# Kernel optimization log

Hardware: AMD Instinct MI355X
Metric: run time of the kernel (lower is better)

The kernel has to match this reference:

```python
import jax, jax.numpy as jnp
import numpy as np

B, C, H, W = 8, 256, 64, 64
CR = C // 4  # reduced channels for Q/K


def setup_inputs() -> dict:
    key = jax.random.key(0)
    ks = jax.random.split(key, 6)
    return {
        "source": jax.random.normal(ks[0], (B, C, H, W), dtype=jnp.float32),
        "guidance": jax.random.normal(ks[1], (B, C, H, W), dtype=jnp.float32),
        "Wq": jax.random.normal(ks[2], (CR, C), dtype=jnp.float32) * 0.02,
        "Wk": jax.random.normal(ks[3], (CR, C), dtype=jnp.float32) * 0.02,
        "Wv": jax.random.normal(ks[4], (C, C), dtype=jnp.float32) * 0.02,
        "bv": jax.random.normal(ks[5], (C,), dtype=jnp.float32) * 0.02,
        "gamma": jnp.zeros((1,), dtype=jnp.float32),
    }


def reference(source, guidance, Wq, Wk, Wv, bv, gamma):
    b, c, h, w = source.shape
    n = h * w
    src = source.reshape(b, c, n)       # [B,C,N]
    gui = guidance.reshape(b, c, n)     # [B,C,N]
    # 1x1 convs == per-pixel linear projections over channels
    Q = jnp.einsum('qc,bcn->bqn', Wq, src)                 # [B,CR,N]
    K = jnp.einsum('qc,bcn->bqn', Wk, gui)                 # [B,CR,N]
    V = jnp.einsum('vc,bcn->bvn', Wv, gui) + bv[None, :, None]  # [B,C,N]
    # energy[b,n,m] = sum_q Q[b,q,n] K[b,q,m]  (unscaled)
    energy = jnp.einsum('bqn,bqm->bnm', Q, K)              # [B,N,N]
    attn = jax.nn.softmax(energy, axis=-1)                 # softmax over keys m
    # out[b,c,n] = sum_m V[b,c,m] attn[b,n,m]
    out = jnp.einsum('bcm,bnm->bcn', V, attn)              # [B,C,N]
    return gamma[0] * out.reshape(b, c, h, w) + source
```

## Files before the change

kernel.cpp:

```cpp
#include <hip/hip_runtime.h>
#include <hip/hip_bf16.h>
#include <stdint.h>


#define B_ 8
#define C_ 256
#define N_ 4096
#define CR_ 64

typedef unsigned short u16;
typedef __attribute__((ext_vector_type(8))) __bf16 bf16x8;
typedef __attribute__((ext_vector_type(4))) float f32x4;
typedef __attribute__((ext_vector_type(16))) float f32x16;

__device__ __forceinline__ u16 f2bf(float f) {
  union { float f; unsigned int u; } v; v.f = f;
  unsigned int r = (v.u + 0x7fffu + ((v.u >> 16) & 1u)) >> 16;
  return (u16)r;
}
__device__ __forceinline__ unsigned int cvtpk(float a, float b) {
  unsigned int r;
  asm("v_cvt_pk_bf16_f32 %0, %1, %2" : "=v"(r) : "v"(a), "v"(b));
  return r;
}

typedef __attribute__((address_space(1))) const unsigned int gu32_t;
typedef __attribute__((address_space(3))) unsigned int lu32_t;
__device__ __forceinline__ void gll16(const void* g, void* l) {
  __builtin_amdgcn_global_load_lds((gu32_t*)g, (lu32_t*)l, 16, 0, 0);
}

__global__ __launch_bounds__(256) void wprep_kernel(
    const float* __restrict__ Wq, const float* __restrict__ Wk,
    const float* __restrict__ Wv, u16* __restrict__ Wb)
{
  const int i = (blockIdx.x * 256 + threadIdx.x) * 4;
  const int row = i >> 8;
  float4 v;
  float s = 1.0f;
  if (row < 64)       { v = *(const float4*)(Wq + i); s = 1.44269504f; }
  else if (row < 128) { v = *(const float4*)(Wk + i - 64 * 256); }
  else                { v = *(const float4*)(Wv + i - 128 * 256); }
  u16* o = Wb + i;
  o[0] = f2bf(v.x * s); o[1] = f2bf(v.y * s);
  o[2] = f2bf(v.z * s); o[3] = f2bf(v.w * s);
}

#define TSTR 266
#define LOAD_TILE(INP, BB, PX0) do {                                         \
    const int p4_ = (t & 15) * 4, r_ = t >> 4;                               \
    const float* ip_ = (INP) + (size_t)(BB) * C_ * N_ + (PX0) + p4_;         \
    for (int k = 0; k < 16; ++k) {                                           \
      const int c_ = r_ + k * 16;                                            \
      float4 v_ = *(const float4*)(ip_ + (size_t)c_ * N_);                   \
      Tl[(p4_ + 0) * TSTR + c_] = f2bf(v_.x);                                \
      Tl[(p4_ + 1) * TSTR + c_] = f2bf(v_.y);                                \
      Tl[(p4_ + 2) * TSTR + c_] = f2bf(v_.z);                                \
      Tl[(p4_ + 3) * TSTR + c_] = f2bf(v_.w);                                \
    }                                                                        \
  } while (0)

__global__ __launch_bounds__(256) void projqkv_kernel(
    const float* __restrict__ src, const float* __restrict__ gui,
    const u16* __restrict__ Wb, const float* __restrict__ bv,
    u16* __restrict__ Qb, u16* __restrict__ Kb, u16* __restrict__ VF)
{
  __shared__ u16 Tl[64 * TSTR];
  const int t = threadIdx.x, lane = t & 63, wave = t >> 6;
  const int lg = lane >> 4, lm = lane & 15;
  const int b = blockIdx.y;
  const int l31 = lane & 31, hi2 = lane >> 5;
  const f32x4 z4 = {0.f, 0.f, 0.f, 0.f};

  if (blockIdx.z == 0) {
    LOAD_TILE(src, b, blockIdx.x * 64);
    __syncthreads();

    f32x4 acc[4];
#pragma unroll
    for (int i = 0; i < 4; ++i) acc[i] = z4;
    for (int ks = 0; ks < 8; ++ks) {
      bf16x8 wf = *(const bf16x8*)(Wb + (wave * 16 + lm) * C_ + ks * 32 + lg * 8);
#pragma unroll
      for (int ni = 0; ni < 4; ++ni) {
        bf16x8 pf = *(const bf16x8*)(&Tl[(ni * 16 + lm) * TSTR + ks * 32 + lg * 8]);
        acc[ni] = __builtin_amdgcn_mfma_f32_16x16x32_bf16(wf, pf, acc[ni], 0, 0, 0);
      }
    }
    __syncthreads();
#pragma unroll
    for (int ni = 0; ni < 4; ++ni)
#pragma unroll
      for (int rp = 0; rp < 2; ++rp)
        *(unsigned int*)&Tl[(ni * 16 + lm) * 72 + wave * 16 + lg * 4 + rp * 2] =
            cvtpk(acc[ni][rp * 2], acc[ni][rp * 2 + 1]);
    __syncthreads();
    u16* op = Qb + (size_t)(b * 64 + blockIdx.x) * 4096 + lane * 8;
#pragma unroll
    for (int fi = 0; fi < 2; ++fi) {
      const int f = wave * 2 + fi, sub = f >> 2, db = f & 3;
      *(uint4*)(op + f * 512) =
          *(const uint4*)(&Tl[(sub * 32 + l31) * 72 + db * 16 + hi2 * 8]);
    }
  } else {
    LOAD_TILE(gui, b, blockIdx.x * 64);
    __syncthreads();

    const u16* Wk64 = Wb + 64 * 256;
    const u16* Wv0  = Wb + 128 * 256 + (size_t)(wave * 64) * 256;
    f32x4 acck[4];
    f32x4 accv[4][4];
#pragma unroll
    for (int i = 0; i < 4; ++i) {
      acck[i] = z4;
#pragma unroll
      for (int j = 0; j < 4; ++j) accv[i][j] = z4;
    }

    for (int ks = 0; ks < 8; ++ks) {
      bf16x8 pf[4];
#pragma unroll
      for (int ni = 0; ni < 4; ++ni)
        pf[ni] = *(const bf16x8*)(&Tl[(ni * 16 + lm) * TSTR + ks * 32 + lg * 8]);
      bf16x8 kwf = *(const bf16x8*)(Wk64 + (wave * 16 + lm) * C_ + ks * 32 + lg * 8);
#pragma unroll
      for (int ni = 0; ni < 4; ++ni)
        acck[ni] = __builtin_amdgcn_mfma_f32_16x16x32_bf16(kwf, pf[ni], acck[ni], 0, 0, 0);
#pragma unroll
      for (int mi = 0; mi < 4; ++mi) {
        bf16x8 vwf = *(const bf16x8*)(Wv0 + (mi * 16 + lm) * C_ + ks * 32 + lg * 8);
#pragma unroll
        for (int ni = 0; ni < 4; ++ni)
          accv[mi][ni] = __builtin_amdgcn_mfma_f32_16x16x32_bf16(vwf, pf[ni], accv[mi][ni], 0, 0, 0);
      }
    }

    f32x4 bq[4];
#pragma unroll
    for (int mi = 0; mi < 4; ++mi)
      bq[mi] = *(const f32x4*)(bv + wave * 64 + mi * 16 + lg * 4);

    __syncthreads();

    u16* tw = Tl + wave * 32 * 72;
    const int half = wave >> 1;
    u16* vo = VF + (((size_t)(b * 64 + blockIdx.x)) * 2 + half) * 8192;
#pragma unroll
    for (int vh = 0; vh < 2; ++vh) {
#pragma unroll
      for (int mi = 0; mi < 2; ++mi)
#pragma unroll
        for (int ni = 0; ni < 4; ++ni)
#pragma unroll
          for (int r = 0; r < 4; ++r)
            tw[(mi * 16 + lg * 4 + r) * 72 + ni * 16 + lm] =
                f2bf(accv[vh * 2 + mi][ni][r] + bq[vh * 2 + mi][r]);
      const int cf = (wave & 1) * 2 + vh;
#pragma unroll
      for (int kblk = 0; kblk < 4; ++kblk)
        *(uint4*)(vo + (cf * 4 + kblk) * 512 + lane * 8) =
            *(const uint4*)(&tw[l31 * 72 + kblk * 16 + hi2 * 8]);
    }

    __syncthreads();
#pragma unroll
    for (int ni = 0; ni < 4; ++ni)
#pragma unroll
      for (int rp = 0; rp < 2; ++rp)
        *(unsigned int*)&Tl[(ni * 16 + lm) * 72 + wave * 16 + lg * 4 + rp * 2] =
            cvtpk(acck[ni][rp * 2], acck[ni][rp * 2 + 1]);
    __syncthreads();
    u16* op = Kb + (size_t)(b * 64 + blockIdx.x) * 4096 + lane * 8;
#pragma unroll
    for (int fi = 0; fi < 2; ++fi) {
      const int f = wave * 2 + fi, sub = f >> 2, db = f & 3;
      *(uint4*)(op + f * 512) =
          *(const uint4*)(&Tl[(sub * 32 + l31) * 72 + db * 16 + hi2 * 8]);
    }
  }
}

#define VB1 16384
#define PB  32768

__global__ __launch_bounds__(256, 4) void attn_kernel(
    const u16* __restrict__ Qb, const u16* __restrict__ Kb, const u16* __restrict__ VF,
    const float* __restrict__ source, const float* __restrict__ gamma,
    float* __restrict__ out)
{
  __shared__ uint4 smem4[2560];
  char* smem = (char*)smem4;

  const int bid = blockIdx.x;
  const int b = bid & 7;
  const int idx = bid >> 3;
  const int qt = idx & 63;
  const int half = idx >> 6;

  const int t = threadIdx.x;
  const int lane = t & 63;
  const int wave = t >> 6;
  const int qw = wave & 1;
  const int wc = wave >> 1;
  const int l31 = lane & 31;
  const int hi = lane >> 5;
  const int q0 = qt * 64;

  bf16x8 aq[4];
  {
    const u16* qp = Qb + ((size_t)(b * 64 + qt)) * 4096 + (qw * 4) * 512 + lane * 8;
#pragma unroll
    for (int db = 0; db < 4; ++db) aq[db] = *(const bf16x8*)(qp + db * 512);
  }

  const u16* KbT = Kb + (size_t)b * (64 * 4096);
  const char* VFb = (const char*)VF + ((size_t)(b * 128 + half)) * 16384;

  f32x16 acc[2];
#pragma unroll
  for (int c2 = 0; c2 < 2; ++c2)
#pragma unroll
    for (int r = 0; r < 16; ++r) acc[c2][r] = 0.f;
  float lpart = 0.f;

  bf16x8 kC[4];
  char* pmy0 = smem + PB + (size_t)((qw * 4 + wc * 2 + 0) << 10) + lane * 16;
  char* pmy1 = smem + PB + (size_t)((qw * 4 + wc * 2 + 1) << 10) + lane * 16;
  const char* pfr0 = smem + PB + (size_t)((qw * 4 + (1 - wc) * 2 + 0) << 10) + lane * 16;
  const char* pfr1 = smem + PB + (size_t)((qw * 4 + (1 - wc) * 2 + 1) << 10) + lane * 16;

#define STAGEV(KTILE, VOFF) do {                                             \
    const char* vs_ = VFb + (size_t)(KTILE) * 32768 + t * 16;                \
    _Pragma("unroll")                                                        \
    for (int i = 0; i < 4; ++i)                                              \
      gll16(vs_ + i * 4096, smem + (VOFF) + wave * 1024 + i * 4096);         \
  } while (0)

#define LOADK(KT) do {                                                       \
    const u16* kp_ = KbT + (size_t)(KT) * 4096 + wc * 2048 + lane * 8;       \
    _Pragma("unroll")                                                        \
    for (int f = 0; f < 4; ++f)                                              \
      kC[f] = *(const bf16x8*)(kp_ + f * 512);                               \
  } while (0)

#define PACK(SF, O8, DST) do {                                               \
    unsigned uA_ = cvtpk(SF[(O8) + 0], SF[(O8) + 1]);                        \
    unsigned vA_ = cvtpk(SF[(O8) + 2], SF[(O8) + 3]);                        \
    unsigned uB_ = cvtpk(SF[(O8) + 4], SF[(O8) + 5]);                        \
    unsigned vB_ = cvtpk(SF[(O8) + 6], SF[(O8) + 7]);                        \
    asm("v_permlane32_swap_b32 %0, %1" : "+v"(uA_), "+v"(uB_));              \
    asm("v_permlane32_swap_b32 %0, %1" : "+v"(vA_), "+v"(vB_));              \
    uint4 pw_; pw_.x = uA_; pw_.y = vA_; pw_.z = uB_; pw_.w = vB_;           \
    __builtin_memcpy(&(DST), &pw_, 16);                                      \
  } while (0)

#define PVK(KBLK, PB8, VCUR) do {                                            \
    __builtin_amdgcn_s_setprio(1);                                           \
    _Pragma("unroll")                                                        \
    for (int c2 = 0; c2 < 2; ++c2) {                                         \
      bf16x8 vf_ = *(const bf16x8*)(smem + (VCUR) +                          \
          (((wc * 2 + c2) * 4 + (KBLK)) << 10) + lane * 16);                 \
      acc[c2] = __builtin_amdgcn_mfma_f32_32x32x16_bf16(vf_, PB8, acc[c2], 0, 0, 0); \
    }                                                                        \
    __builtin_amdgcn_s_setprio(0);                                           \
  } while (0)

#define ITER(KT, VCUR, VNXT) do {                                            \
    __syncthreads();                                                         \
    const int ktn_ = (KT) + 1;                                               \
    const bool ok_ = ktn_ < 64;                                              \
    if (ok_) STAGEV(ktn_, VNXT);                                             \
    f32x16 sf;                                                               \
    _Pragma("unroll")                                                        \
    for (int r = 0; r < 16; ++r) sf[r] = 0.f;                                \
    __builtin_amdgcn_s_setprio(1);                                           \
    _Pragma("unroll")                                                        \
    for (int db = 0; db < 4; ++db)                                           \
      sf = __builtin_amdgcn_mfma_f32_32x32x16_bf16(kC[db], aq[db], sf, 0, 0, 0); \
    __builtin_amdgcn_s_setprio(0);                                           \
    if (ok_) LOADK(ktn_);                                                    \
    float s_ = 0.f;                                                          \
    _Pragma("unroll")                                                        \
    for (int r = 0; r < 16; ++r) {                                           \
      float e_ = __builtin_amdgcn_exp2f(sf[r]);                              \
      sf[r] = e_;                                                            \
      s_ += e_;                                                              \
    }                                                                        \
    lpart += s_;                                                             \
    bf16x8 pf0_, pf1_;                                                       \
    PACK(sf, 0, pf0_);                                                       \
    PACK(sf, 8, pf1_);                                                       \
    *(uint4*)pmy0 = *(const uint4*)&pf0_;                                    \
    *(uint4*)pmy1 = *(const uint4*)&pf1_;                                    \
    asm volatile("s_waitcnt lgkmcnt(0)" ::: "memory");                       \
    __builtin_amdgcn_s_barrier();                                            \
    __builtin_amdgcn_sched_barrier(0);                                       \
    bf16x8 pfa_ = *(const bf16x8*)pfr0;                                      \
    bf16x8 pfb_ = *(const bf16x8*)pfr1;                                      \
    PVK(wc * 2 + 0, pf0_, VCUR);                                             \
    PVK(wc * 2 + 1, pf1_, VCUR);                                             \
    PVK((1 - wc) * 2 + 0, pfa_, VCUR);                                       \
    PVK((1 - wc) * 2 + 1, pfb_, VCUR);                                       \
  } while (0)

  STAGEV(0, 0);
  LOADK(0);
  for (int kt2 = 0; kt2 < 64; kt2 += 2) {
    ITER(kt2,     0,   VB1);
    ITER(kt2 + 1, VB1, 0);
  }
  asm volatile("s_waitcnt vmcnt(0)" ::: "memory");

  float xs = lpart, ys = lpart;
  asm("v_permlane32_swap_b32 %0, %1" : "+v"(xs), "+v"(ys));
  float lhalf = xs + ys;
  __syncthreads();
  *(float*)(smem + PB + (size_t)(((qw * 2 + wc) * 64 + lane) << 2)) = lhalf;
  __syncthreads();
  float lrow = lhalf +
      *(const float*)(smem + PB + (size_t)(((qw * 2 + (1 - wc)) * 64 + lane) << 2));

  const float inv = gamma[0] / fmaxf(lrow, 1e-37f);
#pragma unroll
  for (int c2 = 0; c2 < 2; ++c2)
#pragma unroll
    for (int r = 0; r < 16; ++r) {
      const int ch = half * 128 + wc * 64 + c2 * 32 + (r & 3) + 8 * (r >> 2) + 4 * hi;
      size_t gi = ((size_t)(b * C_ + ch)) * N_ + q0 + qw * 32 + l31;
      out[gi] = acc[c2][r] * inv + source[gi];
    }
}

extern "C" void kernel_launch(void* const* d_in, const int* in_sizes, int n_in,
                              void* d_out, int out_size, void* d_ws, size_t ws_size,
                              hipStream_t stream) {
  const float* src = (const float*)d_in[0];
  const float* gui = (const float*)d_in[1];
  const float* Wq  = (const float*)d_in[2];
  const float* Wk  = (const float*)d_in[3];
  const float* Wv  = (const float*)d_in[4];
  const float* bv  = (const float*)d_in[5];
  const float* gm  = (const float*)d_in[6];
  float* out = (float*)d_out;

  u16* Qb = (u16*)d_ws;
  u16* Kb = Qb + (size_t)B_ * N_ * CR_;
  u16* VF = Kb + (size_t)B_ * N_ * CR_;

  u16* Wb = (u16*)d_out;

  wprep_kernel<<<dim3(96), dim3(256), 0, stream>>>(Wq, Wk, Wv, Wb);
  projqkv_kernel<<<dim3(64, B_, 2), dim3(256), 0, stream>>>(src, gui, Wb, bv, Qb, Kb, VF);
  attn_kernel<<<dim3(1024), dim3(256), 0, stream>>>(Qb, Kb, VF, src, gm, out);
}
```

Measured before the change: 155.0 us.

## Split PV over keys per wave instead of channels, removing per-iteration P exchange

```diff
diff --git a/kernel.cpp b/kernel.cpp
--- a/kernel.cpp
+++ b/kernel.cpp
@@ -181,14 +181,14 @@
 }
 
 #define VB1 16384
-#define PB  32768
-
-__global__ __launch_bounds__(256, 4) void attn_kernel(
+#define LRO 32768
+
+__global__ __launch_bounds__(256, 3) void attn_kernel(
     const u16* __restrict__ Qb, const u16* __restrict__ Kb, const u16* __restrict__ VF,
     const float* __restrict__ source, const float* __restrict__ gamma,
     float* __restrict__ out)
 {
-  __shared__ uint4 smem4[2560];
+  __shared__ uint4 smem4[2080];
   char* smem = (char*)smem4;
 
   const int bid = blockIdx.x;
@@ -216,18 +216,14 @@
   const u16* KbT = Kb + (size_t)b * (64 * 4096);
   const char* VFb = (const char*)VF + ((size_t)(b * 128 + half)) * 16384;
 
-  f32x16 acc[2];
-#pragma unroll
-  for (int c2 = 0; c2 < 2; ++c2)
-#pragma unroll
-    for (int r = 0; r < 16; ++r) acc[c2][r] = 0.f;
+  f32x16 acc[4];
+#pragma unroll
+  for (int cf = 0; cf < 4; ++cf)
+#pragma unroll
+    for (int r = 0; r < 16; ++r) acc[cf][r] = 0.f;
   float lpart = 0.f;
 
   bf16x8 kC[4];
-  char* pmy0 = smem + PB + (size_t)((qw * 4 + wc * 2 + 0) << 10) + lane * 16;
-  char* pmy1 = smem + PB + (size_t)((qw * 4 + wc * 2 + 1) << 10) + lane * 16;
-  const char* pfr0 = smem + PB + (size_t)((qw * 4 + (1 - wc) * 2 + 0) << 10) + lane * 16;
-  const char* pfr1 = smem + PB + (size_t)((qw * 4 + (1 - wc) * 2 + 1) << 10) + lane * 16;
 
 #define STAGEV(KTILE, VOFF) do {                                             \
     const char* vs_ = VFb + (size_t)(KTILE) * 32768 + t * 16;                \
@@ -254,13 +250,13 @@
     __builtin_memcpy(&(DST), &pw_, 16);                                      \
   } while (0)
 
-#define PVK(KBLK, PB8, VCUR) do {                                            \
+#define PVK(KB, PB8, VCUR) do {                                              \
     __builtin_amdgcn_s_setprio(1);                                           \
     _Pragma("unroll")                                                        \
-    for (int c2 = 0; c2 < 2; ++c2) {                                         \
+    for (int cf = 0; cf < 4; ++cf) {                                         \
       bf16x8 vf_ = *(const bf16x8*)(smem + (VCUR) +                          \
-          (((wc * 2 + c2) * 4 + (KBLK)) << 10) + lane * 16);                 \
-      acc[c2] = __builtin_amdgcn_mfma_f32_32x32x16_bf16(vf_, PB8, acc[c2], 0, 0, 0); \
+          (((cf * 4) + (wc * 2 + (KB))) << 10) + lane * 16);                 \
+      acc[cf] = __builtin_amdgcn_mfma_f32_32x32x16_bf16(vf_, PB8, acc[cf], 0, 0, 0); \
     }                                                                        \
     __builtin_amdgcn_s_setprio(0);                                           \
   } while (0)
@@ -290,17 +286,8 @@
     bf16x8 pf0_, pf1_;                                                       \
     PACK(sf, 0, pf0_);                                                       \
     PACK(sf, 8, pf1_);                                                       \
-    *(uint4*)pmy0 = *(const uint4*)&pf0_;                                    \
-    *(uint4*)pmy1 = *(const uint4*)&pf1_;                                    \
-    asm volatile("s_waitcnt lgkmcnt(0)" ::: "memory");                       \
-    __builtin_amdgcn_s_barrier();                                            \
-    __builtin_amdgcn_sched_barrier(0);                                       \
-    bf16x8 pfa_ = *(const bf16x8*)pfr0;                                      \
-    bf16x8 pfb_ = *(const bf16x8*)pfr1;                                      \
-    PVK(wc * 2 + 0, pf0_, VCUR);                                             \
-    PVK(wc * 2 + 1, pf1_, VCUR);                                             \
-    PVK((1 - wc) * 2 + 0, pfa_, VCUR);                                       \
-    PVK((1 - wc) * 2 + 1, pfb_, VCUR);                                       \
+    PVK(0, pf0_, VCUR);                                                      \
+    PVK(1, pf1_, VCUR);                                                      \
   } while (0)
 
   STAGEV(0, 0);
@@ -314,21 +301,41 @@
   float xs = lpart, ys = lpart;
   asm("v_permlane32_swap_b32 %0, %1" : "+v"(xs), "+v"(ys));
   float lhalf = xs + ys;
+
   __syncthreads();
-  *(float*)(smem + PB + (size_t)(((qw * 2 + wc) * 64 + lane) << 2)) = lhalf;
+  char* mb = smem + qw * 16384;
+  if (wc == 1) {
+#pragma unroll
+    for (int cf = 0; cf < 4; ++cf)
+#pragma unroll
+      for (int ck = 0; ck < 4; ++ck) {
+        f32x4 w4;
+#pragma unroll
+        for (int j = 0; j < 4; ++j) w4[j] = acc[cf][ck * 4 + j];
+        *(f32x4*)(mb + ((cf * 4 + ck) << 10) + lane * 16) = w4;
+      }
+    *(float*)(smem + LRO + ((qw * 64 + lane) << 2)) = lhalf;
+  }
   __syncthreads();
-  float lrow = lhalf +
-      *(const float*)(smem + PB + (size_t)(((qw * 2 + (1 - wc)) * 64 + lane) << 2));
-
-  const float inv = gamma[0] / fmaxf(lrow, 1e-37f);
-#pragma unroll
-  for (int c2 = 0; c2 < 2; ++c2)
-#pragma unroll
-    for (int r = 0; r < 16; ++r) {
-      const int ch = half * 128 + wc * 64 + c2 * 32 + (r & 3) + 8 * (r >> 2) + 4 * hi;
-      size_t gi = ((size_t)(b * C_ + ch)) * N_ + q0 + qw * 32 + l31;
-      out[gi] = acc[c2][r] * inv + source[gi];
-    }
+  if (wc == 0) {
+    const float lrow = lhalf + *(const float*)(smem + LRO + ((qw * 64 + lane) << 2));
+    const float inv = gamma[0] / fmaxf(lrow, 1e-37f);
+#pragma unroll
+    for (int cf = 0; cf < 4; ++cf) {
+#pragma unroll
+      for (int ck = 0; ck < 4; ++ck) {
+        f32x4 p4 = *(const f32x4*)(mb + ((cf * 4 + ck) << 10) + lane * 16);
+#pragma unroll
+        for (int j = 0; j < 4; ++j) acc[cf][ck * 4 + j] += p4[j];
+      }
+#pragma unroll
+      for (int r = 0; r < 16; ++r) {
+        const int ch = half * 128 + cf * 32 + (r & 3) + 8 * (r >> 2) + 4 * hi;
+        size_t gi = ((size_t)(b * C_ + ch)) * N_ + q0 + qw * 32 + l31;
+        out[gi] = acc[cf][r] * inv + source[gi];
+      }
+    }
+  }
 }
 
 extern "C" void kernel_launch(void* const* d_in, const int* in_sizes, int n_in,
```

After: 154.3 us. No clear change (-0.5%).
